# Optimization experiments

Measured on AMD Instinct MI355X. Metric: run time of the kernel, lower is better.

The kernel has to match this reference:

```python
import jax, jax.numpy as jnp
import numpy as np

E = 8          # num_experts
TOP_K = 2
D = 1024       # hidden_size
I_MOE = 1024   # moe_intermediate_size (per-expert)
I_SH = 4096    # intermediate_size (shared expert)


def setup_inputs() -> dict:
    key = jax.random.key(0)
    ks = jax.random.split(key, 9)
    s = 0.02
    return {
        "hidden_states": jax.random.normal(ks[0], (2, 4096, D), dtype=jnp.float32),
        "gate_w": jax.random.normal(ks[1], (D, E), dtype=jnp.float32) * s,
        "eg": jax.random.normal(ks[2], (E, D, I_MOE), dtype=jnp.float32) * s,  # gate_proj per expert
        "eu": jax.random.normal(ks[3], (E, D, I_MOE), dtype=jnp.float32) * s,  # up_proj per expert
        "ed": jax.random.normal(ks[4], (E, I_MOE, D), dtype=jnp.float32) * s,  # down_proj per expert
        "sg": jax.random.normal(ks[5], (D, I_SH), dtype=jnp.float32) * s,
        "su": jax.random.normal(ks[6], (D, I_SH), dtype=jnp.float32) * s,
        "sd": jax.random.normal(ks[7], (I_SH, D), dtype=jnp.float32) * s,
        "shared_gate_w": jax.random.normal(ks[8], (D, 1), dtype=jnp.float32) * s,
    }


def _swiglu(x, wg, wu, wd):
    # down_proj(silu(gate_proj(x)) * up_proj(x))
    return (jax.nn.silu(x @ wg) * (x @ wu)) @ wd


def reference(hidden_states, gate_w, eg, eu, ed, sg, su, sd, shared_gate_w):
    B, S, Dm = hidden_states.shape
    x = hidden_states.reshape(-1, Dm)                     # [T, D]

    router_logits = x @ gate_w                            # [T, E]
    probs = jax.nn.softmax(router_logits.astype(jnp.float32), axis=-1)
    topw, topi = jax.lax.top_k(probs, TOP_K)              # [T, K]
    topw = topw / jnp.clip(jnp.sum(topw, axis=-1, keepdims=True), 1e-6)
    topw = topw.astype(x.dtype)

    # combine[t, e] = routing weight of expert e for token t (0 if unselected)
    combine = jnp.sum(jax.nn.one_hot(topi, E, dtype=x.dtype) * topw[..., None], axis=1)  # [T, E]

    out = jnp.zeros_like(x)
    for e in range(E):  # fixed small expert loop (structurally distinct weights)
        out = out + combine[:, e:e + 1] * _swiglu(x, eg[e], eu[e], ed[e])

    shared = _swiglu(x, sg, su, sd)
    shared_gate = jax.nn.sigmoid(x @ shared_gate_w)       # [T, 1]
    out = out + shared_gate * shared

    return out.reshape(B, S, Dm), router_logits
```

## Files before the change

### kernel.cpp

```cpp
#include <hip/hip_runtime.h>
#include <hip/hip_bf16.h>
#include <stdint.h>

#define T_TOK 8192
#define DDIM 1024
#define NEXP 8
#define IMOE 1024
#define ISH 4096
#define BK 64
#define PADTOT 17408

typedef __attribute__((ext_vector_type(8))) short short8;
typedef __attribute__((ext_vector_type(8))) __bf16 bf16x8;
typedef __attribute__((ext_vector_type(4))) float floatx4;

__device__ __forceinline__ unsigned short f2bf(float f) {
  union { float f; unsigned u; } v; v.f = f;
  unsigned r = v.u + 0x7fffu + ((v.u >> 16) & 1u);
  return (unsigned short)(r >> 16);
}

__device__ __forceinline__ floatx4 mfma16(short8 a, short8 b, floatx4 c) {
  return __builtin_amdgcn_mfma_f32_16x16x32_bf16(
      __builtin_bit_cast(bf16x8, a), __builtin_bit_cast(bf16x8, b), c, 0, 0, 0);
}

__device__ __forceinline__ void gload16(const void* g, void* l) {
  __builtin_amdgcn_global_load_lds((const __attribute__((address_space(1))) void*)g,
                                   (__attribute__((address_space(3))) void*)l, 16, 0, 0);
}



__global__ void k_cast(const float* __restrict__ src, unsigned short* __restrict__ dst, int n) {
  int i = (blockIdx.x * blockDim.x + threadIdx.x) * 4;
  if (i < n) {
    float4 v = *(const float4*)(src + i);
    ushort4 o;
    o.x = f2bf(v.x); o.y = f2bf(v.y); o.z = f2bf(v.z); o.w = f2bf(v.w);
    *(ushort4*)(dst + i) = o;
  }
}

__global__ void k_transpose_cast(const float* __restrict__ src, unsigned short* __restrict__ dst,
                                 int R, int C) {
  __shared__ float tile[32][33];
  int b = blockIdx.z;
  int c0 = blockIdx.x * 32, r0 = blockIdx.y * 32;
  const float* s = src + (size_t)b * R * C;
  unsigned short* d = dst + (size_t)b * R * C;
  int tx = threadIdx.x, ty = threadIdx.y;
#pragma unroll
  for (int j = 0; j < 32; j += 8)
    tile[ty + j][tx] = s[(size_t)(r0 + ty + j) * C + c0 + tx];
  __syncthreads();
#pragma unroll
  for (int j = 0; j < 32; j += 8)
    d[(size_t)(c0 + ty + j) * R + r0 + tx] = f2bf(tile[tx][ty + j]);
}


__global__ void k_router(const float* __restrict__ x, const float* __restrict__ gw,
                         const float* __restrict__ sgw, float* __restrict__ logits_out,
                         int* __restrict__ topi, float* __restrict__ topw,
                         float* __restrict__ sgate) {
  int wave = threadIdx.x >> 6;
  int lane = threadIdx.x & 63;
  int t = blockIdx.x * 4 + wave;
  const float* xr = x + (size_t)t * DDIM;
  float acc[9];
#pragma unroll
  for (int j = 0; j < 9; j++) acc[j] = 0.f;
  for (int d = lane; d < DDIM; d += 64) {
    float xv = xr[d];
    const float* g = gw + d * 8;
    float4 g0 = *(const float4*)g;
    float4 g1 = *(const float4*)(g + 4);
    acc[0] += xv * g0.x; acc[1] += xv * g0.y; acc[2] += xv * g0.z; acc[3] += xv * g0.w;
    acc[4] += xv * g1.x; acc[5] += xv * g1.y; acc[6] += xv * g1.z; acc[7] += xv * g1.w;
    acc[8] += xv * sgw[d];
  }
#pragma unroll
  for (int off = 32; off > 0; off >>= 1) {
#pragma unroll
    for (int j = 0; j < 9; j++) acc[j] += __shfl_xor(acc[j], off);
  }
  if (lane == 0) {
#pragma unroll
    for (int j = 0; j < 8; j++) logits_out[t * 8 + j] = acc[j];
    int i0 = 0;
#pragma unroll
    for (int j = 1; j < 8; j++) if (acc[j] > acc[i0]) i0 = j;
    int i1 = -1;
#pragma unroll
    for (int j = 0; j < 8; j++) {
      if (j == i0) continue;
      if (i1 < 0 || acc[j] > acc[i1]) i1 = j;
    }
    float e1 = expf(acc[i1] - acc[i0]);
    float inv = 1.f / (1.f + e1);
    topi[t * 2] = i0; topi[t * 2 + 1] = i1;
    topw[t * 2] = inv; topw[t * 2 + 1] = e1 * inv;
    sgate[t] = 1.f / (1.f + expf(-acc[8]));
  }
}

__global__ void k_hist(const int* __restrict__ topi, int* __restrict__ blockhist) {
  __shared__ int h[NEXP];
  if (threadIdx.x < NEXP) h[threadIdx.x] = 0;
  __syncthreads();
  int i = blockIdx.x * 256 + threadIdx.x;
  atomicAdd(&h[topi[i]], 1);
  __syncthreads();
  if (threadIdx.x < NEXP) blockhist[blockIdx.x * NEXP + threadIdx.x] = h[threadIdx.x];
}

__global__ void k_offsets(const int* __restrict__ blockhist, int* __restrict__ pseg,
                          int* __restrict__ rcnt, int* __restrict__ blockbase) {
  if (threadIdx.x == 0) {
    int tot[NEXP];
#pragma unroll
    for (int e = 0; e < NEXP; e++) tot[e] = 0;
    for (int b = 0; b < 64; b++)
      for (int e = 0; e < NEXP; e++) {
        blockbase[b * NEXP + e] = tot[e];
        tot[e] += blockhist[b * NEXP + e];
      }
    int s = 0;
    for (int e = 0; e < NEXP; e++) {
      rcnt[e] = tot[e];
      pseg[e] = s;
      s += (tot[e] + 127) & ~127;
    }
    pseg[NEXP] = s;
    for (int b = 0; b < 64; b++)
      for (int e = 0; e < NEXP; e++) blockbase[b * NEXP + e] += pseg[e];
  }
}

__global__ void k_scatter(const int* __restrict__ topi, const float* __restrict__ topw,
                          const int* __restrict__ blockbase,
                          int* __restrict__ ptok, float* __restrict__ pw) {
  __shared__ int cur[NEXP];
  if (threadIdx.x < NEXP) cur[threadIdx.x] = blockbase[blockIdx.x * NEXP + threadIdx.x];
  __syncthreads();
  int i = blockIdx.x * 256 + threadIdx.x;
  int e = topi[i];
  int pos = atomicAdd(&cur[e], 1);
  ptok[pos] = i >> 1;
  pw[pos] = topw[i];
}

__global__ void k_gather(const unsigned short* __restrict__ xb, const int* __restrict__ ptok,
                         unsigned short* __restrict__ xg) {
  int row = blockIdx.x * 2 + (threadIdx.x >> 7);
  int col = (threadIdx.x & 127) * 8;
  int tok = ptok[row];
  uint4 v = make_uint4(0, 0, 0, 0);
  if (tok >= 0 && tok < T_TOK) v = *(const uint4*)(xb + (size_t)tok * DDIM + col);
  *(uint4*)(xg + (size_t)row * DDIM + col) = v;
}

__global__ __launch_bounds__(256, 4) void k_gu_shared(
    const unsigned short* __restrict__ Xb,
    const unsigned short* __restrict__ BgT,
    const unsigned short* __restrict__ BuT,
    unsigned short* __restrict__ H)
{
  __shared__ __align__(16) unsigned short As[128 * BK];
  __shared__ __align__(16) unsigned short Bgs[64 * BK];
  __shared__ __align__(16) unsigned short Bus[64 * BK];

  const int tm0 = blockIdx.x * 128;
  const int tn0 = blockIdx.y * 64;
  const int tid = threadIdx.x;
  const int wave = tid >> 6, lane = tid & 63;
  const int wm = wave & 1, wn = wave >> 1;
  const int quad = lane >> 4, l16 = lane & 15;
  const int srow = lane >> 3;
  const int scol = ((lane & 7) ^ srow) * 8;

  floatx4 accg[4][2] = {};
  floatx4 accu[4][2] = {};

  for (int k0 = 0; k0 < DDIM; k0 += BK) {
#pragma unroll
    for (int s = 0; s < 4; s++) {
      int rb = (wave * 4 + s) * 8;
      gload16(Xb + (size_t)(tm0 + rb + srow) * DDIM + k0 + scol, As + rb * BK);
    }
#pragma unroll
    for (int s = 0; s < 2; s++) {
      int rb = (wave * 2 + s) * 8;
      gload16(BgT + (size_t)(tn0 + rb + srow) * DDIM + k0 + scol, Bgs + rb * BK);
      gload16(BuT + (size_t)(tn0 + rb + srow) * DDIM + k0 + scol, Bus + rb * BK);
    }
    __syncthreads();
#pragma unroll
    for (int ks = 0; ks < BK; ks += 32) {
      short8 af[4], bg[2], bu[2];
#pragma unroll
      for (int f = 0; f < 4; f++) {
        int r = wm * 64 + f * 16 + l16;
        af[f] = *(const short8*)(As + r * BK + ((((ks >> 3) + quad) ^ (r & 7)) << 3));
      }
#pragma unroll
      for (int f = 0; f < 2; f++) {
        int r = wn * 32 + f * 16 + l16;
        int off = r * BK + ((((ks >> 3) + quad) ^ (r & 7)) << 3);
        bg[f] = *(const short8*)(Bgs + off);
        bu[f] = *(const short8*)(Bus + off);
      }
#pragma unroll
      for (int fm = 0; fm < 4; fm++)
#pragma unroll
        for (int fn = 0; fn < 2; fn++) {
          accg[fm][fn] = mfma16(af[fm], bg[fn], accg[fm][fn]);
          accu[fm][fn] = mfma16(af[fm], bu[fn], accu[fm][fn]);
        }
    }
    __syncthreads();
  }
#pragma unroll
  for (int fm = 0; fm < 4; fm++)
#pragma unroll
    for (int reg = 0; reg < 4; reg++) {
      int r = tm0 + wm * 64 + fm * 16 + quad * 4 + reg;
#pragma unroll
      for (int fn = 0; fn < 2; fn++) {
        int c = tn0 + wn * 32 + fn * 16 + l16;
        float g = accg[fm][fn][reg];
        float u = accu[fm][fn][reg];
        float h = (g / (1.f + __expf(-g))) * u;
        H[(size_t)r * ISH + c] = f2bf(h);
      }
    }
}

__global__ __launch_bounds__(256, 4) void k_gu_expert(
    const unsigned short* __restrict__ Xg,
    const unsigned short* __restrict__ EgT,
    const unsigned short* __restrict__ EuT,
    const int* __restrict__ pseg,
    unsigned short* __restrict__ Hp)
{
  const int m0 = blockIdx.x * 128;
  if (m0 >= pseg[NEXP]) return;
  int e = 0;
#pragma unroll
  for (int j = 1; j < NEXP; j++) if (m0 >= pseg[j]) e = j;

  __shared__ __align__(16) unsigned short As[128 * BK];
  __shared__ __align__(16) unsigned short Bgs[64 * BK];
  __shared__ __align__(16) unsigned short Bus[64 * BK];

  const int tn0 = blockIdx.y * 64;
  const int tid = threadIdx.x;
  const int wave = tid >> 6, lane = tid & 63;
  const int wm = wave & 1, wn = wave >> 1;
  const int quad = lane >> 4, l16 = lane & 15;
  const int srow = lane >> 3;
  const int scol = ((lane & 7) ^ srow) * 8;

  const unsigned short* Bg = EgT + (size_t)e * IMOE * DDIM;
  const unsigned short* Bu = EuT + (size_t)e * IMOE * DDIM;

  floatx4 accg[4][2] = {};
  floatx4 accu[4][2] = {};

  for (int k0 = 0; k0 < DDIM; k0 += BK) {
#pragma unroll
    for (int s = 0; s < 4; s++) {
      int rb = (wave * 4 + s) * 8;
      gload16(Xg + (size_t)(m0 + rb + srow) * DDIM + k0 + scol, As + rb * BK);
    }
#pragma unroll
    for (int s = 0; s < 2; s++) {
      int rb = (wave * 2 + s) * 8;
      gload16(Bg + (size_t)(tn0 + rb + srow) * DDIM + k0 + scol, Bgs + rb * BK);
      gload16(Bu + (size_t)(tn0 + rb + srow) * DDIM + k0 + scol, Bus + rb * BK);
    }
    __syncthreads();
#pragma unroll
    for (int ks = 0; ks < BK; ks += 32) {
      short8 af[4], bg[2], bu[2];
#pragma unroll
      for (int f = 0; f < 4; f++) {
        int r = wm * 64 + f * 16 + l16;
        af[f] = *(const short8*)(As + r * BK + ((((ks >> 3) + quad) ^ (r & 7)) << 3));
      }
#pragma unroll
      for (int f = 0; f < 2; f++) {
        int r = wn * 32 + f * 16 + l16;
        int off = r * BK + ((((ks >> 3) + quad) ^ (r & 7)) << 3);
        bg[f] = *(const short8*)(Bgs + off);
        bu[f] = *(const short8*)(Bus + off);
      }
#pragma unroll
      for (int fm = 0; fm < 4; fm++)
#pragma unroll
        for (int fn = 0; fn < 2; fn++) {
          accg[fm][fn] = mfma16(af[fm], bg[fn], accg[fm][fn]);
          accu[fm][fn] = mfma16(af[fm], bu[fn], accu[fm][fn]);
        }
    }
    __syncthreads();
  }
#pragma unroll
  for (int fm = 0; fm < 4; fm++)
#pragma unroll
    for (int reg = 0; reg < 4; reg++) {
      int r = m0 + wm * 64 + fm * 16 + quad * 4 + reg;
#pragma unroll
      for (int fn = 0; fn < 2; fn++) {
        int c = tn0 + wn * 32 + fn * 16 + l16;
        float g = accg[fm][fn][reg];
        float u = accu[fm][fn][reg];
        Hp[(size_t)r * IMOE + c] = f2bf((g / (1.f + __expf(-g))) * u);
      }
    }
}

__global__ __launch_bounds__(256, 4) void k_down_shared(
    const unsigned short* __restrict__ Hsh,
    const unsigned short* __restrict__ SdT,
    const float* __restrict__ sgate,
    float* __restrict__ out)
{
  __shared__ __align__(16) unsigned short As[128 * BK];
  __shared__ __align__(16) unsigned short Bs[128 * BK];

  const int tm0 = blockIdx.x * 128;
  const int tn0 = blockIdx.y * 128;
  const int tid = threadIdx.x;
  const int wave = tid >> 6, lane = tid & 63;
  const int wm = wave & 1, wn = wave >> 1;
  const int quad = lane >> 4, l16 = lane & 15;
  const int srow = lane >> 3;
  const int scol = ((lane & 7) ^ srow) * 8;

  floatx4 acc[4][4] = {};

  for (int k0 = 0; k0 < ISH; k0 += BK) {
#pragma unroll
    for (int s = 0; s < 4; s++) {
      int rb = (wave * 4 + s) * 8;
      gload16(Hsh + (size_t)(tm0 + rb + srow) * ISH + k0 + scol, As + rb * BK);
      gload16(SdT + (size_t)(tn0 + rb + srow) * ISH + k0 + scol, Bs + rb * BK);
    }
    __syncthreads();
#pragma unroll
    for (int ks = 0; ks < BK; ks += 32) {
      short8 af[4], bfr[4];
#pragma unroll
      for (int f = 0; f < 4; f++) {
        int ra = wm * 64 + f * 16 + l16;
        int rb2 = wn * 64 + f * 16 + l16;
        af[f] = *(const short8*)(As + ra * BK + ((((ks >> 3) + quad) ^ (ra & 7)) << 3));
        bfr[f] = *(const short8*)(Bs + rb2 * BK + ((((ks >> 3) + quad) ^ (rb2 & 7)) << 3));
      }
#pragma unroll
      for (int fm = 0; fm < 4; fm++)
#pragma unroll
        for (int fn = 0; fn < 4; fn++)
          acc[fm][fn] = mfma16(af[fm], bfr[fn], acc[fm][fn]);
    }
    __syncthreads();
  }
#pragma unroll
  for (int fm = 0; fm < 4; fm++)
#pragma unroll
    for (int reg = 0; reg < 4; reg++) {
      int r = tm0 + wm * 64 + fm * 16 + quad * 4 + reg;
      float gt = sgate[r];
#pragma unroll
      for (int fn = 0; fn < 4; fn++) {
        int c = tn0 + wn * 64 + fn * 16 + l16;
        out[(size_t)r * DDIM + c] = gt * acc[fm][fn][reg];
      }
    }
}

__global__ __launch_bounds__(256, 4) void k_down_expert(
    const unsigned short* __restrict__ Hp,
    const unsigned short* __restrict__ EdT,
    const int* __restrict__ pseg,
    const int* __restrict__ rcnt,
    const int* __restrict__ ptok,
    const float* __restrict__ pw,
    float* __restrict__ out)
{
  const int m0 = blockIdx.x * 128;
  if (m0 >= pseg[NEXP]) return;
  int e = 0;
#pragma unroll
  for (int j = 1; j < NEXP; j++) if (m0 >= pseg[j]) e = j;
  const int sbase = pseg[e];
  const int cnt = rcnt[e];

  __shared__ __align__(16) unsigned short As[128 * BK];
  __shared__ __align__(16) unsigned short Bs[128 * BK];

  const int tn0 = blockIdx.y * 128;
  const int tid = threadIdx.x;
  const int wave = tid >> 6, lane = tid & 63;
  const int wm = wave & 1, wn = wave >> 1;
  const int quad = lane >> 4, l16 = lane & 15;
  const int srow = lane >> 3;
  const int scol = ((lane & 7) ^ srow) * 8;

  const unsigned short* B = EdT + (size_t)e * IMOE * DDIM;

  floatx4 acc[4][4] = {};

  for (int k0 = 0; k0 < IMOE; k0 += BK) {
#pragma unroll
    for (int s = 0; s < 4; s++) {
      int rb = (wave * 4 + s) * 8;
      gload16(Hp + (size_t)(m0 + rb + srow) * IMOE + k0 + scol, As + rb * BK);
      gload16(B + (size_t)(tn0 + rb + srow) * IMOE + k0 + scol, Bs + rb * BK);
    }
    __syncthreads();
#pragma unroll
    for (int ks = 0; ks < BK; ks += 32) {
      short8 af[4], bfr[4];
#pragma unroll
      for (int f = 0; f < 4; f++) {
        int ra = wm * 64 + f * 16 + l16;
        int rb2 = wn * 64 + f * 16 + l16;
        af[f] = *(const short8*)(As + ra * BK + ((((ks >> 3) + quad) ^ (ra & 7)) << 3));
        bfr[f] = *(const short8*)(Bs + rb2 * BK + ((((ks >> 3) + quad) ^ (rb2 & 7)) << 3));
      }
#pragma unroll
      for (int fm = 0; fm < 4; fm++)
#pragma unroll
        for (int fn = 0; fn < 4; fn++)
          acc[fm][fn] = mfma16(af[fm], bfr[fn], acc[fm][fn]);
    }
    __syncthreads();
  }
#pragma unroll
  for (int fm = 0; fm < 4; fm++)
#pragma unroll
    for (int reg = 0; reg < 4; reg++) {
      int grow = m0 + wm * 64 + fm * 16 + quad * 4 + reg;
      if (grow - sbase < cnt) {
        int t = ptok[grow];
        float w = pw[grow];
#pragma unroll
        for (int fn = 0; fn < 4; fn++) {
          int c = tn0 + wn * 64 + fn * 16 + l16;
          atomicAdd(&out[(size_t)t * DDIM + c], w * acc[fm][fn][reg]);
        }
      }
    }
}


extern "C" void kernel_launch(void* const* d_in, const int* in_sizes, int n_in,
                              void* d_out, int out_size, void* d_ws, size_t ws_size,
                              hipStream_t stream) {
  const float* x   = (const float*)d_in[0];
  const float* gw  = (const float*)d_in[1];
  const float* eg  = (const float*)d_in[2];
  const float* eu  = (const float*)d_in[3];
  const float* ed  = (const float*)d_in[4];
  const float* sg  = (const float*)d_in[5];
  const float* su  = (const float*)d_in[6];
  const float* sd  = (const float*)d_in[7];
  const float* sgw = (const float*)d_in[8];

  float* out    = (float*)d_out;
  float* logits = out + (size_t)T_TOK * DDIM;

  char* ws = (char*)d_ws;
  unsigned short* xb   = (unsigned short*)(ws + 0);
  unsigned short* egT  = (unsigned short*)(ws + 16777216);
  unsigned short* euT  = (unsigned short*)(ws + 33554432);
  unsigned short* edT  = (unsigned short*)(ws + 50331648);
  unsigned short* sgT  = (unsigned short*)(ws + 67108864);
  unsigned short* suT  = (unsigned short*)(ws + 75497472);
  unsigned short* sdT  = (unsigned short*)(ws + 83886080);
  unsigned short* hsh  = (unsigned short*)(ws + 92274688);
  unsigned short* xg   = (unsigned short*)(ws + 92274688);
  unsigned short* hp   = (unsigned short*)(ws + 159383552);
  int*   topi      = (int*)  (ws + 195035136);
  float* topw      = (float*)(ws + 195100672);
  float* sgate     = (float*)(ws + 195166208);
  int*   ptok      = (int*)  (ws + 195198976);
  float* pw        = (float*)(ws + 195268608);
  int*   blockhist = (int*)  (ws + 195338240);
  int*   blockbase = (int*)  (ws + 195340288);
  int*   pseg      = (int*)  (ws + 195342336);
  int*   rcnt      = (int*)  (ws + 195342400);

  k_cast<<<8192, 256, 0, stream>>>(x, xb, T_TOK * DDIM);
  k_transpose_cast<<<dim3(32, 32, 8), dim3(32, 8), 0, stream>>>(eg, egT, DDIM, IMOE);
  k_transpose_cast<<<dim3(32, 32, 8), dim3(32, 8), 0, stream>>>(eu, euT, DDIM, IMOE);
  k_transpose_cast<<<dim3(32, 32, 8), dim3(32, 8), 0, stream>>>(ed, edT, IMOE, DDIM);
  k_transpose_cast<<<dim3(128, 32, 1), dim3(32, 8), 0, stream>>>(sg, sgT, DDIM, ISH);
  k_transpose_cast<<<dim3(128, 32, 1), dim3(32, 8), 0, stream>>>(su, suT, DDIM, ISH);
  k_transpose_cast<<<dim3(32, 128, 1), dim3(32, 8), 0, stream>>>(sd, sdT, ISH, DDIM);

  k_router<<<T_TOK / 4, 256, 0, stream>>>(x, gw, sgw, logits, topi, topw, sgate);
  k_hist<<<64, 256, 0, stream>>>(topi, blockhist);
  k_offsets<<<1, 64, 0, stream>>>(blockhist, pseg, rcnt, blockbase);
  k_scatter<<<64, 256, 0, stream>>>(topi, topw, blockbase, ptok, pw);
  k_gather<<<PADTOT / 2, 256, 0, stream>>>(xb, ptok, xg);

  k_gu_expert<<<dim3(PADTOT / 128, 16), 256, 0, stream>>>(xg, egT, euT, pseg, hp);
  k_gu_shared<<<dim3(64, 64), 256, 0, stream>>>(xb, sgT, suT, hsh);
  k_down_shared<<<dim3(64, 8), 256, 0, stream>>>(hsh, sdT, sgate, out);
  k_down_expert<<<dim3(PADTOT / 128, 8), 256, 0, stream>>>(hp, edT, pseg, rcnt, ptok, pw, out);

  (void)in_sizes; (void)n_in; (void)out_size; (void)ws_size;
}
```

Before: 685.5 us.

## Fuse cast into router, gather into expert GEMM, merge transposes, shrink down tiles

The fp32-to-bf16 cast of the activations moves into the router kernel, and the separate gather kernel is removed. The expert gate/up GEMM now loads token rows through ptok-indexed pointers instead. The six transpose-cast launches are merged into three. Both down-projection kernels go from 128-wide to 64-wide N tiles, doubling their grids, and the launch order is changed. This cuts launches and extra HBM passes, at the cost of smaller down-GEMM tiles that lower data reuse.

```diff
diff --git a/kernel.cpp b/kernel.cpp
--- a/kernel.cpp
+++ b/kernel.cpp
@@ -32,23 +32,11 @@
 
 
 
-__global__ void k_cast(const float* __restrict__ src, unsigned short* __restrict__ dst, int n) {
-  int i = (blockIdx.x * blockDim.x + threadIdx.x) * 4;
-  if (i < n) {
-    float4 v = *(const float4*)(src + i);
-    ushort4 o;
-    o.x = f2bf(v.x); o.y = f2bf(v.y); o.z = f2bf(v.z); o.w = f2bf(v.w);
-    *(ushort4*)(dst + i) = o;
-  }
-}
-
-__global__ void k_transpose_cast(const float* __restrict__ src, unsigned short* __restrict__ dst,
-                                 int R, int C) {
+
+__device__ __forceinline__ void tr_cast_body(const float* __restrict__ s,
+                                             unsigned short* __restrict__ d, int R, int C) {
   __shared__ float tile[32][33];
-  int b = blockIdx.z;
   int c0 = blockIdx.x * 32, r0 = blockIdx.y * 32;
-  const float* s = src + (size_t)b * R * C;
-  unsigned short* d = dst + (size_t)b * R * C;
   int tx = threadIdx.x, ty = threadIdx.y;
 #pragma unroll
   for (int j = 0; j < 32; j += 8)
@@ -59,20 +47,41 @@
     d[(size_t)(c0 + ty + j) * R + r0 + tx] = f2bf(tile[tx][ty + j]);
 }
 
+__global__ void k_tr_experts(const float* __restrict__ eg, const float* __restrict__ eu,
+                             const float* __restrict__ ed, unsigned short* __restrict__ egT,
+                             unsigned short* __restrict__ euT, unsigned short* __restrict__ edT) {
+  int z = blockIdx.z, sel = z >> 3, b = z & 7;
+  const float* s = (sel == 0 ? eg : sel == 1 ? eu : ed) + (size_t)b * 1024 * 1024;
+  unsigned short* d = (sel == 0 ? egT : sel == 1 ? euT : edT) + (size_t)b * 1024 * 1024;
+  tr_cast_body(s, d, 1024, 1024);
+}
+
+__global__ void k_tr_su(const float* __restrict__ sg, const float* __restrict__ su,
+                        unsigned short* __restrict__ sgT, unsigned short* __restrict__ suT) {
+  if (blockIdx.z == 0) tr_cast_body(sg, sgT, DDIM, ISH);
+  else                 tr_cast_body(su, suT, DDIM, ISH);
+}
+
+__global__ void k_tr_sd(const float* __restrict__ sd, unsigned short* __restrict__ sdT) {
+  tr_cast_body(sd, sdT, ISH, DDIM);
+}
+
 
 __global__ void k_router(const float* __restrict__ x, const float* __restrict__ gw,
                          const float* __restrict__ sgw, float* __restrict__ logits_out,
                          int* __restrict__ topi, float* __restrict__ topw,
-                         float* __restrict__ sgate) {
+                         float* __restrict__ sgate, unsigned short* __restrict__ xb) {
   int wave = threadIdx.x >> 6;
   int lane = threadIdx.x & 63;
   int t = blockIdx.x * 4 + wave;
   const float* xr = x + (size_t)t * DDIM;
+  unsigned short* xbr = xb + (size_t)t * DDIM;
   float acc[9];
 #pragma unroll
   for (int j = 0; j < 9; j++) acc[j] = 0.f;
   for (int d = lane; d < DDIM; d += 64) {
     float xv = xr[d];
+    xbr[d] = f2bf(xv);
     const float* g = gw + d * 8;
     float4 g0 = *(const float4*)g;
     float4 g1 = *(const float4*)(g + 4);
@@ -151,15 +160,6 @@
   pw[pos] = topw[i];
 }
 
-__global__ void k_gather(const unsigned short* __restrict__ xb, const int* __restrict__ ptok,
-                         unsigned short* __restrict__ xg) {
-  int row = blockIdx.x * 2 + (threadIdx.x >> 7);
-  int col = (threadIdx.x & 127) * 8;
-  int tok = ptok[row];
-  uint4 v = make_uint4(0, 0, 0, 0);
-  if (tok >= 0 && tok < T_TOK) v = *(const uint4*)(xb + (size_t)tok * DDIM + col);
-  *(uint4*)(xg + (size_t)row * DDIM + col) = v;
-}
 
 __global__ __launch_bounds__(256, 4) void k_gu_shared(
     const unsigned short* __restrict__ Xb,
@@ -167,9 +167,178 @@
     const unsigned short* __restrict__ BuT,
     unsigned short* __restrict__ H)
 {
+  const int tm0 = blockIdx.x * 128;
+  const int tn0 = blockIdx.y * 64;
+
   __shared__ __align__(16) unsigned short As[128 * BK];
   __shared__ __align__(16) unsigned short Bgs[64 * BK];
   __shared__ __align__(16) unsigned short Bus[64 * BK];
+
+  const int tid = threadIdx.x;
+  const int wave = tid >> 6, lane = tid & 63;
+  const int wm = wave & 1, wn = wave >> 1;
+  const int quad = lane >> 4, l16 = lane & 15;
+  const int srow = lane >> 3;
+  const int scol = ((lane & 7) ^ srow) * 8;
+
+  floatx4 accg[4][2] = {};
+  floatx4 accu[4][2] = {};
+
+  for (int k0 = 0; k0 < DDIM; k0 += BK) {
+#pragma unroll
+    for (int s = 0; s < 4; s++) {
+      int rb = (wave * 4 + s) * 8;
+      gload16(Xb + (size_t)(tm0 + rb + srow) * DDIM + k0 + scol, As + rb * BK);
+    }
+#pragma unroll
+    for (int s = 0; s < 2; s++) {
+      int rb = (wave * 2 + s) * 8;
+      gload16(BgT + (size_t)(tn0 + rb + srow) * DDIM + k0 + scol, Bgs + rb * BK);
+      gload16(BuT + (size_t)(tn0 + rb + srow) * DDIM + k0 + scol, Bus + rb * BK);
+    }
+    __syncthreads();
+#pragma unroll
+    for (int ks = 0; ks < BK; ks += 32) {
+      short8 af[4], bg[2], bu[2];
+#pragma unroll
+      for (int f = 0; f < 4; f++) {
+        int r = wm * 64 + f * 16 + l16;
+        af[f] = *(const short8*)(As + r * BK + ((((ks >> 3) + quad) ^ (r & 7)) << 3));
+      }
+#pragma unroll
+      for (int f = 0; f < 2; f++) {
+        int r = wn * 32 + f * 16 + l16;
+        int off = r * BK + ((((ks >> 3) + quad) ^ (r & 7)) << 3);
+        bg[f] = *(const short8*)(Bgs + off);
+        bu[f] = *(const short8*)(Bus + off);
+      }
+#pragma unroll
+      for (int fm = 0; fm < 4; fm++)
+#pragma unroll
+        for (int fn = 0; fn < 2; fn++) {
+          accg[fm][fn] = mfma16(af[fm], bg[fn], accg[fm][fn]);
+          accu[fm][fn] = mfma16(af[fm], bu[fn], accu[fm][fn]);
+        }
+    }
+    __syncthreads();
+  }
+#pragma unroll
+  for (int fm = 0; fm < 4; fm++)
+#pragma unroll
+    for (int reg = 0; reg < 4; reg++) {
+      int r = tm0 + wm * 64 + fm * 16 + quad * 4 + reg;
+#pragma unroll
+      for (int fn = 0; fn < 2; fn++) {
+        int c = tn0 + wn * 32 + fn * 16 + l16;
+        float g = accg[fm][fn][reg];
+        float u = accu[fm][fn][reg];
+        float h = (g / (1.f + __expf(-g))) * u;
+        H[(size_t)r * ISH + c] = f2bf(h);
+      }
+    }
+}
+
+__global__ __launch_bounds__(256, 4) void k_gu_expert(
+    const unsigned short* __restrict__ Xb,
+    const unsigned short* __restrict__ EgT,
+    const unsigned short* __restrict__ EuT,
+    const int* __restrict__ pseg,
+    const int* __restrict__ ptok,
+    unsigned short* __restrict__ Hp)
+{
+  const int m0 = blockIdx.x * 128;
+  if (m0 >= pseg[NEXP]) return;
+  int e = 0;
+#pragma unroll
+  for (int j = 1; j < NEXP; j++) if (m0 >= pseg[j]) e = j;
+
+  __shared__ __align__(16) unsigned short As[128 * BK];
+  __shared__ __align__(16) unsigned short Bgs[64 * BK];
+  __shared__ __align__(16) unsigned short Bus[64 * BK];
+
+  const int tn0 = blockIdx.y * 64;
+  const int tid = threadIdx.x;
+  const int wave = tid >> 6, lane = tid & 63;
+  const int wm = wave & 1, wn = wave >> 1;
+  const int quad = lane >> 4, l16 = lane & 15;
+  const int srow = lane >> 3;
+  const int scol = ((lane & 7) ^ srow) * 8;
+
+  const unsigned short* Bg = EgT + (size_t)e * IMOE * DDIM;
+  const unsigned short* Bu = EuT + (size_t)e * IMOE * DDIM;
+
+  const unsigned short* ArowP[4];
+#pragma unroll
+  for (int s = 0; s < 4; s++) {
+    int tok = ptok[m0 + (wave * 4 + s) * 8 + srow];
+    if (tok < 0 || tok >= T_TOK) tok = 0;
+    ArowP[s] = Xb + (size_t)tok * DDIM + scol;
+  }
+
+  floatx4 accg[4][2] = {};
+  floatx4 accu[4][2] = {};
+
+  for (int k0 = 0; k0 < DDIM; k0 += BK) {
+#pragma unroll
+    for (int s = 0; s < 4; s++) {
+      int rb = (wave * 4 + s) * 8;
+      gload16(ArowP[s] + k0, As + rb * BK);
+    }
+#pragma unroll
+    for (int s = 0; s < 2; s++) {
+      int rb = (wave * 2 + s) * 8;
+      gload16(Bg + (size_t)(tn0 + rb + srow) * DDIM + k0 + scol, Bgs + rb * BK);
+      gload16(Bu + (size_t)(tn0 + rb + srow) * DDIM + k0 + scol, Bus + rb * BK);
+    }
+    __syncthreads();
+#pragma unroll
+    for (int ks = 0; ks < BK; ks += 32) {
+      short8 af[4], bg[2], bu[2];
+#pragma unroll
+      for (int f = 0; f < 4; f++) {
+        int r = wm * 64 + f * 16 + l16;
+        af[f] = *(const short8*)(As + r * BK + ((((ks >> 3) + quad) ^ (r & 7)) << 3));
+      }
+#pragma unroll
+      for (int f = 0; f < 2; f++) {
+        int r = wn * 32 + f * 16 + l16;
+        int off = r * BK + ((((ks >> 3) + quad) ^ (r & 7)) << 3);
+        bg[f] = *(const short8*)(Bgs + off);
+        bu[f] = *(const short8*)(Bus + off);
+      }
+#pragma unroll
+      for (int fm = 0; fm < 4; fm++)
+#pragma unroll
+        for (int fn = 0; fn < 2; fn++) {
+          accg[fm][fn] = mfma16(af[fm], bg[fn], accg[fm][fn]);
+          accu[fm][fn] = mfma16(af[fm], bu[fn], accu[fm][fn]);
+        }
+    }
+    __syncthreads();
+  }
+#pragma unroll
+  for (int fm = 0; fm < 4; fm++)
+#pragma unroll
+    for (int reg = 0; reg < 4; reg++) {
+      int r = m0 + wm * 64 + fm * 16 + quad * 4 + reg;
+#pragma unroll
+      for (int fn = 0; fn < 2; fn++) {
+        int c = tn0 + wn * 32 + fn * 16 + l16;
+        float g = accg[fm][fn][reg];
+        float u = accu[fm][fn][reg];
+        Hp[(size_t)r * IMOE + c] = f2bf((g / (1.f + __expf(-g))) * u);
+      }
+    }
+}
+
+__global__ __launch_bounds__(256, 4) void k_down_shared(
+    const unsigned short* __restrict__ Hsh,
+    const unsigned short* __restrict__ SdT,
+    const float* __restrict__ sgate,
+    float* __restrict__ out)
+{
+  __shared__ __align__(16) unsigned short As[128 * BK];
+  __shared__ __align__(16) unsigned short Bs[64 * BK];
 
   const int tm0 = blockIdx.x * 128;
   const int tn0 = blockIdx.y * 64;
@@ -180,25 +349,23 @@
   const int srow = lane >> 3;
   const int scol = ((lane & 7) ^ srow) * 8;
 
-  floatx4 accg[4][2] = {};
-  floatx4 accu[4][2] = {};
-
-  for (int k0 = 0; k0 < DDIM; k0 += BK) {
+  floatx4 acc[4][2] = {};
+
+  for (int k0 = 0; k0 < ISH; k0 += BK) {
 #pragma unroll
     for (int s = 0; s < 4; s++) {
       int rb = (wave * 4 + s) * 8;
-      gload16(Xb + (size_t)(tm0 + rb + srow) * DDIM + k0 + scol, As + rb * BK);
+      gload16(Hsh + (size_t)(tm0 + rb + srow) * ISH + k0 + scol, As + rb * BK);
     }
 #pragma unroll
     for (int s = 0; s < 2; s++) {
       int rb = (wave * 2 + s) * 8;
-      gload16(BgT + (size_t)(tn0 + rb + srow) * DDIM + k0 + scol, Bgs + rb * BK);
-      gload16(BuT + (size_t)(tn0 + rb + srow) * DDIM + k0 + scol, Bus + rb * BK);
+      gload16(SdT + (size_t)(tn0 + rb + srow) * ISH + k0 + scol, Bs + rb * BK);
     }
     __syncthreads();
 #pragma unroll
     for (int ks = 0; ks < BK; ks += 32) {
-      short8 af[4], bg[2], bu[2];
+      short8 af[4], bfr[2];
 #pragma unroll
       for (int f = 0; f < 4; f++) {
         int r = wm * 64 + f * 16 + l16;
@@ -207,162 +374,12 @@
 #pragma unroll
       for (int f = 0; f < 2; f++) {
         int r = wn * 32 + f * 16 + l16;
-        int off = r * BK + ((((ks >> 3) + quad) ^ (r & 7)) << 3);
-        bg[f] = *(const short8*)(Bgs + off);
-        bu[f] = *(const short8*)(Bus + off);
+        bfr[f] = *(const short8*)(Bs + r * BK + ((((ks >> 3) + quad) ^ (r & 7)) << 3));
       }
 #pragma unroll
       for (int fm = 0; fm < 4; fm++)
 #pragma unroll
-        for (int fn = 0; fn < 2; fn++) {
-          accg[fm][fn] = mfma16(af[fm], bg[fn], accg[fm][fn]);
-          accu[fm][fn] = mfma16(af[fm], bu[fn], accu[fm][fn]);
-        }
-    }
-    __syncthreads();
-  }
-#pragma unroll
-  for (int fm = 0; fm < 4; fm++)
-#pragma unroll
-    for (int reg = 0; reg < 4; reg++) {
-      int r = tm0 + wm * 64 + fm * 16 + quad * 4 + reg;
-#pragma unroll
-      for (int fn = 0; fn < 2; fn++) {
-        int c = tn0 + wn * 32 + fn * 16 + l16;
-        float g = accg[fm][fn][reg];
-        float u = accu[fm][fn][reg];
-        float h = (g / (1.f + __expf(-g))) * u;
-        H[(size_t)r * ISH + c] = f2bf(h);
-      }
-    }
-}
-
-__global__ __launch_bounds__(256, 4) void k_gu_expert(
-    const unsigned short* __restrict__ Xg,
-    const unsigned short* __restrict__ EgT,
-    const unsigned short* __restrict__ EuT,
-    const int* __restrict__ pseg,
-    unsigned short* __restrict__ Hp)
-{
-  const int m0 = blockIdx.x * 128;
-  if (m0 >= pseg[NEXP]) return;
-  int e = 0;
-#pragma unroll
-  for (int j = 1; j < NEXP; j++) if (m0 >= pseg[j]) e = j;
-
-  __shared__ __align__(16) unsigned short As[128 * BK];
-  __shared__ __align__(16) unsigned short Bgs[64 * BK];
-  __shared__ __align__(16) unsigned short Bus[64 * BK];
-
-  const int tn0 = blockIdx.y * 64;
-  const int tid = threadIdx.x;
-  const int wave = tid >> 6, lane = tid & 63;
-  const int wm = wave & 1, wn = wave >> 1;
-  const int quad = lane >> 4, l16 = lane & 15;
-  const int srow = lane >> 3;
-  const int scol = ((lane & 7) ^ srow) * 8;
-
-  const unsigned short* Bg = EgT + (size_t)e * IMOE * DDIM;
-  const unsigned short* Bu = EuT + (size_t)e * IMOE * DDIM;
-
-  floatx4 accg[4][2] = {};
-  floatx4 accu[4][2] = {};
-
-  for (int k0 = 0; k0 < DDIM; k0 += BK) {
-#pragma unroll
-    for (int s = 0; s < 4; s++) {
-      int rb = (wave * 4 + s) * 8;
-      gload16(Xg + (size_t)(m0 + rb + srow) * DDIM + k0 + scol, As + rb * BK);
-    }
-#pragma unroll
-    for (int s = 0; s < 2; s++) {
-      int rb = (wave * 2 + s) * 8;
-      gload16(Bg + (size_t)(tn0 + rb + srow) * DDIM + k0 + scol, Bgs + rb * BK);
-      gload16(Bu + (size_t)(tn0 + rb + srow) * DDIM + k0 + scol, Bus + rb * BK);
-    }
-    __syncthreads();
-#pragma unroll
-    for (int ks = 0; ks < BK; ks += 32) {
-      short8 af[4], bg[2], bu[2];
-#pragma unroll
-      for (int f = 0; f < 4; f++) {
-        int r = wm * 64 + f * 16 + l16;
-        af[f] = *(const short8*)(As + r * BK + ((((ks >> 3) + quad) ^ (r & 7)) << 3));
-      }
-#pragma unroll
-      for (int f = 0; f < 2; f++) {
-        int r = wn * 32 + f * 16 + l16;
-        int off = r * BK + ((((ks >> 3) + quad) ^ (r & 7)) << 3);
-        bg[f] = *(const short8*)(Bgs + off);
-        bu[f] = *(const short8*)(Bus + off);
-      }
-#pragma unroll
-      for (int fm = 0; fm < 4; fm++)
-#pragma unroll
-        for (int fn = 0; fn < 2; fn++) {
-          accg[fm][fn] = mfma16(af[fm], bg[fn], accg[fm][fn]);
-          accu[fm][fn] = mfma16(af[fm], bu[fn], accu[fm][fn]);
-        }
-    }
-    __syncthreads();
-  }
-#pragma unroll
-  for (int fm = 0; fm < 4; fm++)
-#pragma unroll
-    for (int reg = 0; reg < 4; reg++) {
-      int r = m0 + wm * 64 + fm * 16 + quad * 4 + reg;
-#pragma unroll
-      for (int fn = 0; fn < 2; fn++) {
-        int c = tn0 + wn * 32 + fn * 16 + l16;
-        float g = accg[fm][fn][reg];
-        float u = accu[fm][fn][reg];
-        Hp[(size_t)r * IMOE + c] = f2bf((g / (1.f + __expf(-g))) * u);
-      }
-    }
-}
-
-__global__ __launch_bounds__(256, 4) void k_down_shared(
-    const unsigned short* __restrict__ Hsh,
-    const unsigned short* __restrict__ SdT,
-    const float* __restrict__ sgate,
-    float* __restrict__ out)
-{
-  __shared__ __align__(16) unsigned short As[128 * BK];
-  __shared__ __align__(16) unsigned short Bs[128 * BK];
-
-  const int tm0 = blockIdx.x * 128;
-  const int tn0 = blockIdx.y * 128;
-  const int tid = threadIdx.x;
-  const int wave = tid >> 6, lane = tid & 63;
-  const int wm = wave & 1, wn = wave >> 1;
-  const int quad = lane >> 4, l16 = lane & 15;
-  const int srow = lane >> 3;
-  const int scol = ((lane & 7) ^ srow) * 8;
-
-  floatx4 acc[4][4] = {};
-
-  for (int k0 = 0; k0 < ISH; k0 += BK) {
-#pragma unroll
-    for (int s = 0; s < 4; s++) {
-      int rb = (wave * 4 + s) * 8;
-      gload16(Hsh + (size_t)(tm0 + rb + srow) * ISH + k0 + scol, As + rb * BK);
-      gload16(SdT + (size_t)(tn0 + rb + srow) * ISH + k0 + scol, Bs + rb * BK);
-    }
-    __syncthreads();
-#pragma unroll
-    for (int ks = 0; ks < BK; ks += 32) {
-      short8 af[4], bfr[4];
-#pragma unroll
-      for (int f = 0; f < 4; f++) {
-        int ra = wm * 64 + f * 16 + l16;
-        int rb2 = wn * 64 + f * 16 + l16;
-        af[f] = *(const short8*)(As + ra * BK + ((((ks >> 3) + quad) ^ (ra & 7)) << 3));
-        bfr[f] = *(const short8*)(Bs + rb2 * BK + ((((ks >> 3) + quad) ^ (rb2 & 7)) << 3));
-      }
-#pragma unroll
-      for (int fm = 0; fm < 4; fm++)
-#pragma unroll
-        for (int fn = 0; fn < 4; fn++)
+        for (int fn = 0; fn < 2; fn++)
           acc[fm][fn] = mfma16(af[fm], bfr[fn], acc[fm][fn]);
     }
     __syncthreads();
@@ -374,8 +391,8 @@
       int r = tm0 + wm * 64 + fm * 16 + quad * 4 + reg;
       float gt = sgate[r];
 #pragma unroll
-      for (int fn = 0; fn < 4; fn++) {
-        int c = tn0 + wn * 64 + fn * 16 + l16;
+      for (int fn = 0; fn < 2; fn++) {
+        int c = tn0 + wn * 32 + fn * 16 + l16;
         out[(size_t)r * DDIM + c] = gt * acc[fm][fn][reg];
       }
     }
@@ -399,9 +416,9 @@
   const int cnt = rcnt[e];
 
   __shared__ __align__(16) unsigned short As[128 * BK];
-  __shared__ __align__(16) unsigned short Bs[128 * BK];
-
-  const int tn0 = blockIdx.y * 128;
+  __shared__ __align__(16) unsigned short Bs[64 * BK];
+
+  const int tn0 = blockIdx.y * 64;
   const int tid = threadIdx.x;
   const int wave = tid >> 6, lane = tid & 63;
   const int wm = wave & 1, wn = wave >> 1;
@@ -411,30 +428,37 @@
 
   const unsigned short* B = EdT + (size_t)e * IMOE * DDIM;
 
-  floatx4 acc[4][4] = {};
+  floatx4 acc[4][2] = {};
 
   for (int k0 = 0; k0 < IMOE; k0 += BK) {
 #pragma unroll
     for (int s = 0; s < 4; s++) {
       int rb = (wave * 4 + s) * 8;
       gload16(Hp + (size_t)(m0 + rb + srow) * IMOE + k0 + scol, As + rb * BK);
+    }
+#pragma unroll
+    for (int s = 0; s < 2; s++) {
+      int rb = (wave * 2 + s) * 8;
       gload16(B + (size_t)(tn0 + rb + srow) * IMOE + k0 + scol, Bs + rb * BK);
     }
     __syncthreads();
 #pragma unroll
     for (int ks = 0; ks < BK; ks += 32) {
-      short8 af[4], bfr[4];
+      short8 af[4], bfr[2];
 #pragma unroll
       for (int f = 0; f < 4; f++) {
-        int ra = wm * 64 + f * 16 + l16;
-        int rb2 = wn * 64 + f * 16 + l16;
-        af[f] = *(const short8*)(As + ra * BK + ((((ks >> 3) + quad) ^ (ra & 7)) << 3));
-        bfr[f] = *(const short8*)(Bs + rb2 * BK + ((((ks >> 3) + quad) ^ (rb2 & 7)) << 3));
+        int r = wm * 64 + f * 16 + l16;
+        af[f] = *(const short8*)(As + r * BK + ((((ks >> 3) + quad) ^ (r & 7)) << 3));
+      }
+#pragma unroll
+      for (int f = 0; f < 2; f++) {
+        int r = wn * 32 + f * 16 + l16;
+        bfr[f] = *(const short8*)(Bs + r * BK + ((((ks >> 3) + quad) ^ (r & 7)) << 3));
       }
 #pragma unroll
       for (int fm = 0; fm < 4; fm++)
 #pragma unroll
-        for (int fn = 0; fn < 4; fn++)
+        for (int fn = 0; fn < 2; fn++)
           acc[fm][fn] = mfma16(af[fm], bfr[fn], acc[fm][fn]);
     }
     __syncthreads();
@@ -448,8 +472,8 @@
         int t = ptok[grow];
         float w = pw[grow];
 #pragma unroll
-        for (int fn = 0; fn < 4; fn++) {
-          int c = tn0 + wn * 64 + fn * 16 + l16;
+        for (int fn = 0; fn < 2; fn++) {
+          int c = tn0 + wn * 32 + fn * 16 + l16;
           atomicAdd(&out[(size_t)t * DDIM + c], w * acc[fm][fn][reg]);
         }
       }
@@ -482,7 +506,6 @@
   unsigned short* suT  = (unsigned short*)(ws + 75497472);
   unsigned short* sdT  = (unsigned short*)(ws + 83886080);
   unsigned short* hsh  = (unsigned short*)(ws + 92274688);
-  unsigned short* xg   = (unsigned short*)(ws + 92274688);
   unsigned short* hp   = (unsigned short*)(ws + 159383552);
   int*   topi      = (int*)  (ws + 195035136);
   float* topw      = (float*)(ws + 195100672);
@@ -492,26 +515,21 @@
   int*   blockhist = (int*)  (ws + 195338240);
   int*   blockbase = (int*)  (ws + 195340288);
   int*   pseg      = (int*)  (ws + 195342336);
-  int*   rcnt      = (int*)  (ws + 195342400);
-
-  k_cast<<<8192, 256, 0, stream>>>(x, xb, T_TOK * DDIM);
-  k_transpose_cast<<<dim3(32, 32, 8), dim3(32, 8), 0, stream>>>(eg, egT, DDIM, IMOE);
-  k_transpose_cast<<<dim3(32, 32, 8), dim3(32, 8), 0, stream>>>(eu, euT, DDIM, IMOE);
-  k_transpose_cast<<<dim3(32, 32, 8), dim3(32, 8), 0, stream>>>(ed, edT, IMOE, DDIM);
-  k_transpose_cast<<<dim3(128, 32, 1), dim3(32, 8), 0, stream>>>(sg, sgT, DDIM, ISH);
-  k_transpose_cast<<<dim3(128, 32, 1), dim3(32, 8), 0, stream>>>(su, suT, DDIM, ISH);
-  k_transpose_cast<<<dim3(32, 128, 1), dim3(32, 8), 0, stream>>>(sd, sdT, ISH, DDIM);
-
-  k_router<<<T_TOK / 4, 256, 0, stream>>>(x, gw, sgw, logits, topi, topw, sgate);
+  int*   rcnt     = (int*)  (ws + 195342400);
+
+  k_router<<<T_TOK / 4, 256, 0, stream>>>(x, gw, sgw, logits, topi, topw, sgate, xb);
+  k_tr_experts<<<dim3(32, 32, 24), dim3(32, 8), 0, stream>>>(eg, eu, ed, egT, euT, edT);
+  k_tr_su<<<dim3(128, 32, 2), dim3(32, 8), 0, stream>>>(sg, su, sgT, suT);
+  k_tr_sd<<<dim3(32, 128, 1), dim3(32, 8), 0, stream>>>(sd, sdT);
+
   k_hist<<<64, 256, 0, stream>>>(topi, blockhist);
   k_offsets<<<1, 64, 0, stream>>>(blockhist, pseg, rcnt, blockbase);
   k_scatter<<<64, 256, 0, stream>>>(topi, topw, blockbase, ptok, pw);
-  k_gather<<<PADTOT / 2, 256, 0, stream>>>(xb, ptok, xg);
-
-  k_gu_expert<<<dim3(PADTOT / 128, 16), 256, 0, stream>>>(xg, egT, euT, pseg, hp);
+
   k_gu_shared<<<dim3(64, 64), 256, 0, stream>>>(xb, sgT, suT, hsh);
-  k_down_shared<<<dim3(64, 8), 256, 0, stream>>>(hsh, sdT, sgate, out);
-  k_down_expert<<<dim3(PADTOT / 128, 8), 256, 0, stream>>>(hp, edT, pseg, rcnt, ptok, pw, out);
+  k_down_shared<<<dim3(64, 16), 256, 0, stream>>>(hsh, sdT, sgate, out);
+  k_gu_expert<<<dim3(PADTOT / 128, 16), 256, 0, stream>>>(xb, egT, euT, pseg, ptok, hp);
+  k_down_expert<<<dim3(PADTOT / 128, 16), 256, 0, stream>>>(hp, edT, pseg, rcnt, ptok, pw, out);
 
   (void)in_sizes; (void)n_in; (void)out_size; (void)ws_size;
 }
```

Result: faster. 658.3 us (-4.0%).
